# Kernel optimization log

Hardware: AMD Instinct MI355X
Metric: run time of the kernel (lower is better)

Reference implementation:

```python
import jax, jax.numpy as jnp
import numpy as np
import math

D = 1024      # d_model
K = 64        # k_eigenstates
H = 4         # n_heads
KH = K // H   # eigenstates per head
MLP = 4 * D
B, T = 4, 4096


def setup_inputs() -> dict:
    key = jax.random.key(0)
    ks = jax.random.split(key, 16)
    rn = lambda k, shape, s: (jax.random.normal(k, shape, jnp.float32) * s)
    inp = {
        "x": rn(ks[0], (B, T, D), 1.0),
        "W_in": rn(ks[1], (2 * K, D), 1.0 / math.sqrt(D)),
        "log_decay": jax.random.uniform(ks[2], (K,), jnp.float32, -3.0, -0.1),
        "frequency": jnp.linspace(0.0, 2 * math.pi * (1 - 1.0 / K), K, dtype=jnp.float32),
        "W_sel": rn(ks[3], (2 * K, D), 0.01 / math.sqrt(D)),
        "b_sel": jnp.zeros((2 * K,), jnp.float32),
        "R": jnp.eye(KH, dtype=jnp.float32)[None] + 0.01 * rn(ks[4], (H, KH, KH), 1.0 / math.sqrt(KH)),
        "W_out": rn(ks[5], (D, 2 * K), 1.0 / math.sqrt(2 * K)),
        "W_g": rn(ks[6], (D, D), 1.0 / math.sqrt(D)),
        "b_g": jnp.full((D,), -2.0, jnp.float32),
        "g1": jnp.ones((D,), jnp.float32),
        "be1": jnp.zeros((D,), jnp.float32),
        "g2": jnp.ones((D,), jnp.float32),
        "be2": jnp.zeros((D,), jnp.float32),
        "W1": rn(ks[7], (MLP, D), 1.0 / math.sqrt(D)),
        "b1": jnp.zeros((MLP,), jnp.float32),
        "W2": rn(ks[8], (D, MLP), 1.0 / math.sqrt(MLP)),
        "b2": jnp.zeros((D,), jnp.float32),
    }
    return inp


def _ln(x, g, b):
    m = jnp.mean(x, axis=-1, keepdims=True)
    v = jnp.mean(jnp.square(x - m), axis=-1, keepdims=True)
    return (x - m) * jax.lax.rsqrt(v + 1e-5) * g + b


def _scan_combine(e1, e2):
    a1, b1 = e1
    a2, b2 = e2
    return a1 * a2, a2 * b1 + b2


def reference(x, W_in, log_decay, frequency, W_sel, b_sel, R, W_out, W_g, b_g,
              g1, be1, g2, be2, W1, b1, W2, b2):
    Bsz, Ts, Dm = x.shape
    residual = x
    x_norm = _ln(x, g1, be1)

    beta = x_norm @ W_in.T                      # [B,T,2K]
    beta_r, beta_i = jnp.split(beta, 2, axis=-1)

    delta = x_norm @ W_sel.T + b_sel            # selective modulation
    d_dec, d_fr = jnp.split(delta, 2, axis=-1)
    mag = jax.nn.sigmoid(log_decay + 0.1 * jnp.tanh(d_dec))   # [B,T,K]
    freq = frequency + 0.05 * jnp.tanh(d_fr)

    a = jax.lax.complex(mag * jnp.cos(freq), mag * jnp.sin(freq))  # lambda_t
    bc = jax.lax.complex(beta_r, beta_i)
    # inclusive prefix scan of c_t = a_t * c_{t-1} + b_t
    _, c = jax.lax.associative_scan(_scan_combine, (a, bc), axis=1)
    c_r, c_i = c.real, c.imag                   # [B,T,K]

    nH, Kh = R.shape[0], R.shape[1]
    c_r = jnp.einsum('hjk,bthk->bthj', R, c_r.reshape(Bsz, Ts, nH, Kh)).reshape(Bsz, Ts, -1)
    c_i = jnp.einsum('hjk,bthk->bthj', R, c_i.reshape(Bsz, Ts, nH, Kh)).reshape(Bsz, Ts, -1)

    h = jnp.concatenate([c_r, c_i], axis=-1) @ W_out.T
    gate = jax.nn.sigmoid(x_norm @ W_g.T + b_g)
    x = residual + gate * h

    x2 = _ln(x, g2, be2)
    x = x + (jax.nn.silu(x2 @ W1.T + b1) @ W2.T + b2)
    return x
```

## Files before the change

### kernel.cpp

```cpp
#include <hip/hip_runtime.h>
#include <math.h>

typedef __bf16 bf16_t;
typedef __attribute__((ext_vector_type(8))) __bf16 bf16x8;
typedef __attribute__((ext_vector_type(4))) __bf16 bf16x4;
typedef __attribute__((ext_vector_type(4))) float f32x4;

#define DMODEL 1024
#define NROWS  16384
#define SEQLEN 4096

static __device__ __forceinline__ float sigmoidf_(float v) { return 1.f / (1.f + __expf(-v)); }
static __device__ __forceinline__ float tanhf_(float v) {
  v = fminf(fmaxf(v, -15.f), 15.f);
  float e = __expf(-2.f * v);
  return (1.f - e) / (1.f + e);
}

#define GLOAD16(gsrc, ldst) __builtin_amdgcn_global_load_lds(                     \
    (const __attribute__((address_space(1))) void*)(gsrc),                        \
    (__attribute__((address_space(3))) void*)(ldst), 16, 0, 0)

__global__ __launch_bounds__(256) void ln_fused_kernel(const float* __restrict__ x,
                                                       const float* __restrict__ g,
                                                       const float* __restrict__ b,
                                                       bf16_t* __restrict__ out) {
  int row = blockIdx.x;
  int tid = threadIdx.x;
  const float4* xr = (const float4*)(x + (size_t)row * DMODEL);
  float4 v = xr[tid];
  float s  = v.x + v.y + v.z + v.w;
  float s2 = v.x*v.x + v.y*v.y + v.z*v.z + v.w*v.w;
  #pragma unroll
  for (int off = 32; off > 0; off >>= 1) {
    s  += __shfl_down(s, off);
    s2 += __shfl_down(s2, off);
  }
  __shared__ float sh[4], sh2[4];
  int lane = tid & 63, wid = tid >> 6;
  if (lane == 0) { sh[wid] = s; sh2[wid] = s2; }
  __syncthreads();
  s  = sh[0] + sh[1] + sh[2] + sh[3];
  s2 = sh2[0] + sh2[1] + sh2[2] + sh2[3];
  float m = s * (1.f / DMODEL);
  float var = fmaxf(s2 * (1.f / DMODEL) - m * m, 0.f);
  float rs = rsqrtf(var + 1e-5f);
  float4 gv = *(const float4*)&g[tid * 4];
  float4 bv = *(const float4*)&b[tid * 4];
  union { bf16_t h[4]; float2 f2; } u;
  u.h[0] = (bf16_t)((v.x - m) * rs * gv.x + bv.x);
  u.h[1] = (bf16_t)((v.y - m) * rs * gv.y + bv.y);
  u.h[2] = (bf16_t)((v.z - m) * rs * gv.z + bv.z);
  u.h[3] = (bf16_t)((v.w - m) * rs * gv.w + bv.w);
  *(float2*)&out[(size_t)row * DMODEL + tid * 4] = u.f2;
}

__global__ __launch_bounds__(256) void ln_fused_bf16_kernel(const bf16_t* __restrict__ x,
                                                            const float* __restrict__ g,
                                                            const float* __restrict__ b,
                                                            bf16_t* __restrict__ out) {
  int row = blockIdx.x;
  int tid = threadIdx.x;
  bf16x4 hv = *(const bf16x4*)(x + (size_t)row * DMODEL + tid * 4);
  float v0 = (float)hv[0], v1 = (float)hv[1], v2 = (float)hv[2], v3 = (float)hv[3];
  float s  = v0 + v1 + v2 + v3;
  float s2 = v0*v0 + v1*v1 + v2*v2 + v3*v3;
  #pragma unroll
  for (int off = 32; off > 0; off >>= 1) {
    s  += __shfl_down(s, off);
    s2 += __shfl_down(s2, off);
  }
  __shared__ float sh[4], sh2[4];
  int lane = tid & 63, wid = tid >> 6;
  if (lane == 0) { sh[wid] = s; sh2[wid] = s2; }
  __syncthreads();
  s  = sh[0] + sh[1] + sh[2] + sh[3];
  s2 = sh2[0] + sh2[1] + sh2[2] + sh2[3];
  float m = s * (1.f / DMODEL);
  float var = fmaxf(s2 * (1.f / DMODEL) - m * m, 0.f);
  float rs = rsqrtf(var + 1e-5f);
  float4 gv = *(const float4*)&g[tid * 4];
  float4 bv = *(const float4*)&b[tid * 4];
  union { bf16_t h[4]; float2 f2; } u;
  u.h[0] = (bf16_t)((v0 - m) * rs * gv.x + bv.x);
  u.h[1] = (bf16_t)((v1 - m) * rs * gv.y + bv.y);
  u.h[2] = (bf16_t)((v2 - m) * rs * gv.z + bv.z);
  u.h[3] = (bf16_t)((v3 - m) * rs * gv.w + bv.w);
  *(float2*)&out[(size_t)row * DMODEL + tid * 4] = u.f2;
}

__global__ __launch_bounds__(256) void f32_to_bf16_kernel(const float* __restrict__ in,
                                                          bf16_t* __restrict__ out, int n) {
  int idx = (blockIdx.x * 256 + threadIdx.x) * 4;
  if (idx >= n) return;
  float4 v = *(const float4*)&in[idx];
  union { bf16_t h[4]; float2 f2; } u;
  u.h[0] = (bf16_t)v.x; u.h[1] = (bf16_t)v.y; u.h[2] = (bf16_t)v.z; u.h[3] = (bf16_t)v.w;
  *(float2*)&out[idx] = u.f2;
}

template<int EPI>
__global__ __launch_bounds__(512, 4) void gemmB_kernel(
    const bf16_t* __restrict__ A, int lda,
    const bf16_t* __restrict__ B, int ldb, int K, int nx,
    const float* __restrict__ bias,
    const float* __restrict__ resf,
    const bf16_t* __restrict__ resb,
    const bf16_t* __restrict__ auxb,
    float* __restrict__ outf, bf16_t* __restrict__ outb, int ldout) {
  __shared__ __align__(128) bf16_t Asm[128 * 64];
  __shared__ __align__(128) bf16_t Bsm[256 * 64];
  const int nwg = gridDim.x;
  const int bid = blockIdx.x;
  const int lid = (bid & 7) * (nwg >> 3) + (bid >> 3);
  const int n0 = (lid % nx) * 256;
  const int r0 = (lid / nx) * 128;

  const int tid = threadIdx.x;
  const int lane = tid & 63;
  const int w = tid >> 6;
  const int wr = w >> 2, wc = w & 3;
  const int fr = lane & 15;
  const int q16 = (lane >> 4) * 16;
  const int swz = (fr & 7) << 4;
  const int trow = tid >> 3;
  const int scolb = ((tid & 7) ^ (trow & 7)) << 4;

  const size_t lda_b = (size_t)lda * 2;
  const size_t ldb_b = (size_t)ldb * 2;
  const char* Ab = (const char*)A;
  const char* Bb = (const char*)B;
  char* lA = (char*)Asm;
  char* lB = (char*)Bsm;

  f32x4 acc[4][4];
  #pragma unroll
  for (int m = 0; m < 4; ++m)
    #pragma unroll
    for (int n = 0; n < 4; ++n) acc[m][n] = (f32x4){0.f, 0.f, 0.f, 0.f};

  for (int kt = 0; kt < K; kt += 64) {
    const char* sa = Ab + (size_t)(r0 + trow) * lda_b + kt * 2 + scolb;
    GLOAD16(sa, lA + tid * 16);
    GLOAD16(sa + 64 * lda_b, lA + 8192 + tid * 16);
    const char* sb = Bb + (size_t)(n0 + trow) * ldb_b + kt * 2 + scolb;
    GLOAD16(sb, lB + tid * 16);
    GLOAD16(sb + 64 * ldb_b,  lB + 8192  + tid * 16);
    GLOAD16(sb + 128 * ldb_b, lB + 16384 + tid * 16);
    GLOAD16(sb + 192 * ldb_b, lB + 24576 + tid * 16);
    __syncthreads();
    #pragma unroll
    for (int kh = 0; kh < 2; ++kh) {
      bf16x8 af[4], bv[4];
      #pragma unroll
      for (int m = 0; m < 4; ++m)
        af[m] = *(const bf16x8*)(lA + (wr * 64 + m * 16 + fr) * 128 + ((kh * 64 + q16) ^ swz));
      #pragma unroll
      for (int n = 0; n < 4; ++n)
        bv[n] = *(const bf16x8*)(lB + (wc * 64 + n * 16 + fr) * 128 + ((kh * 64 + q16) ^ swz));
      #pragma unroll
      for (int m = 0; m < 4; ++m)
        #pragma unroll
        for (int n = 0; n < 4; ++n)
          acc[m][n] = __builtin_amdgcn_mfma_f32_16x16x32_bf16(af[m], bv[n], acc[m][n], 0, 0, 0);
    }
    __syncthreads();
  }

  const int rbase = (lane >> 4) * 4;
  #pragma unroll
  for (int mf = 0; mf < 4; ++mf) {
    #pragma unroll
    for (int n = 0; n < 4; ++n) {
      int row = r0 + wr * 64 + mf * 16 + rbase;
      int col = n0 + wc * 64 + n * 16 + fr;
      f32x4 v = acc[mf][n];
      #pragma unroll
      for (int j = 0; j < 4; ++j) {
        int r = row + j;
        float val = v[j];
        if (EPI == 0) {
          outf[(size_t)r * ldout + col] = val;
        } else if (EPI == 1) {
          float t2 = val + bias[col];
          t2 = t2 * sigmoidf_(t2);
          outb[(size_t)r * ldout + col] = (bf16_t)t2;
        } else if (EPI == 2) {
          outf[(size_t)r * ldout + col] =
              (float)resb[(size_t)r * 1024 + col] + bias[col] + val;
        } else if (EPI == 3) {
          outf[(size_t)r * ldout + col] += val;
        } else if (EPI == 4) {
          size_t idx = (size_t)r * 1024 + col;
          outb[idx] = (bf16_t)(resf[idx] + sigmoidf_(val + bias[col]) * (float)auxb[idx]);
        } else {
          outb[(size_t)r * ldout + col] = (bf16_t)val;
        }
      }
    }
  }
}

template<int EPI>
__global__ __launch_bounds__(256) void gemm_bf16_kernel(
    const bf16_t* __restrict__ A, int lda,
    const bf16_t* __restrict__ B, int ldb, int K, int nx,
    float* __restrict__ outf, int ldout) {
  __shared__ __align__(16) bf16_t As[128 * 32];
  __shared__ __align__(16) bf16_t Bs[128 * 32];
  const int nwg = gridDim.x;
  const int bid = blockIdx.x;
  const int lid = (bid & 7) * (nwg >> 3) + (bid >> 3);
  const int n0 = (lid % nx) * 128;
  const int r0 = (lid / nx) * 128;

  const int tid = threadIdx.x;
  const int lane = tid & 63;
  const int w = tid >> 6;
  const int wr = w >> 1, wc = w & 1;
  const int srow0 = tid >> 2;
  const int srow1 = 64 + (tid >> 2);
  const int skk = (tid & 3) * 8;
  const int fr = lane & 15;
  const int ko = (lane >> 4) * 8;

  f32x4 acc[4][4];
  #pragma unroll
  for (int m = 0; m < 4; ++m)
    #pragma unroll
    for (int n = 0; n < 4; ++n) acc[m][n] = (f32x4){0.f, 0.f, 0.f, 0.f};

  for (int k0 = 0; k0 < K; k0 += 32) {
    GLOAD16(A + (size_t)(r0 + srow0) * lda + k0 + skk, (char*)As + w * 1024);
    GLOAD16(A + (size_t)(r0 + srow1) * lda + k0 + skk, (char*)As + 4096 + w * 1024);
    GLOAD16(B + (size_t)(n0 + srow0) * ldb + k0 + skk, (char*)Bs + w * 1024);
    GLOAD16(B + (size_t)(n0 + srow1) * ldb + k0 + skk, (char*)Bs + 4096 + w * 1024);
    __syncthreads();
    bf16x8 af[4], bfr[4];
    #pragma unroll
    for (int m = 0; m < 4; ++m)
      af[m] = *(const bf16x8*)&As[(wr * 64 + m * 16 + fr) * 32 + ko];
    #pragma unroll
    for (int n = 0; n < 4; ++n)
      bfr[n] = *(const bf16x8*)&Bs[(wc * 64 + n * 16 + fr) * 32 + ko];
    #pragma unroll
    for (int m = 0; m < 4; ++m)
      #pragma unroll
      for (int n = 0; n < 4; ++n)
        acc[m][n] = __builtin_amdgcn_mfma_f32_16x16x32_bf16(af[m], bfr[n], acc[m][n], 0, 0, 0);
    __syncthreads();
  }

  const int rbase = (lane >> 4) * 4;
  #pragma unroll
  for (int m = 0; m < 4; ++m) {
    #pragma unroll
    for (int n = 0; n < 4; ++n) {
      int row = r0 + wr * 64 + m * 16 + rbase;
      int col = n0 + wc * 64 + n * 16 + fr;
      f32x4 v = acc[m][n];
      #pragma unroll
      for (int j = 0; j < 4; ++j)
        outf[(size_t)(row + j) * ldout + col] = v[j];
    }
  }
}

__global__ __launch_bounds__(256) void scan_fused_kernel(
    const float* __restrict__ bdt,
    const float* __restrict__ log_decay, const float* __restrict__ frequency,
    const float* __restrict__ b_sel,
    float* __restrict__ c_r, float* __restrict__ c_i) {
  int seq = blockIdx.x;
  int bb = seq >> 6, k = seq & 63;
  int tid = threadIdx.x;
  size_t col = (size_t)bb * 4096 + tid * 16;
  const f32x4* pbr = (const f32x4*)(bdt + (size_t)k * 16384 + col);
  const f32x4* pbi = (const f32x4*)(bdt + (size_t)(64 + k) * 16384 + col);
  const f32x4* pdd = (const f32x4*)(bdt + (size_t)(128 + k) * 16384 + col);
  const f32x4* pdf = (const f32x4*)(bdt + (size_t)(192 + k) * 16384 + col);
  const float ld = log_decay[k], fq = frequency[k];
  const float bsd = b_sel[k], bsf = b_sel[64 + k];

  float arv[16], aiv[16], brv[16], biv[16];
  float Ar = 1.f, Ai = 0.f, Br = 0.f, Bi = 0.f;
  #pragma unroll
  for (int g = 0; g < 4; ++g) {
    f32x4 vbr = pbr[g], vbi = pbi[g], vdd = pdd[g], vdf = pdf[g];
    #pragma unroll
    for (int j = 0; j < 4; ++j) {
      int s = g * 4 + j;
      float mag = sigmoidf_(ld + 0.1f * tanhf_(vdd[j] + bsd));
      float f = fq + 0.05f * tanhf_(vdf[j] + bsf);
      float sn, cs;
      __sincosf(f, &sn, &cs);
      float ar = mag * cs, ai = mag * sn;
      float br = vbr[j], bi = vbi[j];
      arv[s] = ar; aiv[s] = ai; brv[s] = br; biv[s] = bi;
      float nBr = ar * Br - ai * Bi + br;
      float nBi = ar * Bi + ai * Br + bi;
      Br = nBr; Bi = nBi;
      float nAr = ar * Ar - ai * Ai;
      float nAi = ar * Ai + ai * Ar;
      Ar = nAr; Ai = nAi;
    }
  }

  __shared__ float sAr[256], sAi[256], sBr[256], sBi[256];
  sAr[tid] = Ar; sAi[tid] = Ai; sBr[tid] = Br; sBi[tid] = Bi;
  for (int off = 1; off < 256; off <<= 1) {
    __syncthreads();
    float pAr = 0.f, pAi = 0.f, pBr = 0.f, pBi = 0.f;
    if (tid >= off) { pAr = sAr[tid - off]; pAi = sAi[tid - off]; pBr = sBr[tid - off]; pBi = sBi[tid - off]; }
    __syncthreads();
    if (tid >= off) {
      float cAr = sAr[tid], cAi = sAi[tid], cBr = sBr[tid], cBi = sBi[tid];
      float nBr = cAr * pBr - cAi * pBi + cBr;
      float nBi = cAr * pBi + cAi * pBr + cBi;
      float nAr = cAr * pAr - cAi * pAi;
      float nAi = cAr * pAi + cAi * pAr;
      sAr[tid] = nAr; sAi[tid] = nAi; sBr[tid] = nBr; sBi[tid] = nBi;
    }
  }
  __syncthreads();
  float cr = (tid > 0) ? sBr[tid - 1] : 0.f;
  float ci = (tid > 0) ? sBi[tid - 1] : 0.f;

  float* outr = c_r + (size_t)seq * 4096 + tid * 16;
  float* outi = c_i + (size_t)seq * 4096 + tid * 16;
  #pragma unroll
  for (int g = 0; g < 4; ++g) {
    f32x4 vr, vi;
    #pragma unroll
    for (int j = 0; j < 4; ++j) {
      int s = g * 4 + j;
      float nr = arv[s] * cr - aiv[s] * ci + brv[s];
      float ni = arv[s] * ci + aiv[s] * cr + biv[s];
      cr = nr; ci = ni;
      vr[j] = cr; vi[j] = ci;
    }
    *(f32x4*)(outr + g * 4) = vr;
    *(f32x4*)(outi + g * 4) = vi;
  }
}

__global__ __launch_bounds__(256) void transpose_cc_kernel(
    const float* __restrict__ c_r, const float* __restrict__ c_i,
    bf16_t* __restrict__ cc) {
  __shared__ float Tr[64][65];
  __shared__ float Ti[64][65];
  int t0 = blockIdx.x * 64;
  int bb = blockIdx.y;
  int tid = threadIdx.x;
  int tt = tid & 63;
  int q = tid >> 6;
  #pragma unroll
  for (int p = 0; p < 16; ++p) {
    int k = p * 4 + q;
    size_t src = ((size_t)bb * 64 + k) * 4096 + t0 + tt;
    Tr[tt][k] = c_r[src];
    Ti[tt][k] = c_i[src];
  }
  __syncthreads();
  #pragma unroll
  for (int p = 0; p < 16; ++p) {
    int tt2 = p * 4 + q;
    int k = tid & 63;
    size_t row = (size_t)bb * 4096 + t0 + tt2;
    cc[row * 128 + k] = (bf16_t)Tr[tt2][k];
    cc[row * 128 + 64 + k] = (bf16_t)Ti[tt2][k];
  }
}

__global__ __launch_bounds__(256) void weff_kernel(const float* __restrict__ W_out,
                                                   const float* __restrict__ R,
                                                   bf16_t* __restrict__ Weff) {
  int idx = blockIdx.x * 256 + threadIdx.x;
  int d = idx >> 7, col = idx & 127;
  int k = col & 63, h = k >> 4, kk = k & 15;
  int off = (col < 64) ? 0 : 64;
  float s = 0.f;
  #pragma unroll
  for (int j = 0; j < 16; ++j)
    s += W_out[d * 128 + off + h * 16 + j] * R[h * 256 + j * 16 + kk];
  Weff[idx] = (bf16_t)s;
}

extern "C" void kernel_launch(void* const* d_in, const int* in_sizes, int n_in,
                              void* d_out, int out_size, void* d_ws, size_t ws_size,
                              hipStream_t stream) {
  (void)in_sizes; (void)n_in; (void)out_size;
  const float* x         = (const float*)d_in[0];
  const float* W_in      = (const float*)d_in[1];
  const float* log_decay = (const float*)d_in[2];
  const float* frequency = (const float*)d_in[3];
  const float* W_sel     = (const float*)d_in[4];
  const float* b_sel     = (const float*)d_in[5];
  const float* R         = (const float*)d_in[6];
  const float* W_out     = (const float*)d_in[7];
  const float* W_g       = (const float*)d_in[8];
  const float* b_g       = (const float*)d_in[9];
  const float* g1        = (const float*)d_in[10];
  const float* be1       = (const float*)d_in[11];
  const float* g2        = (const float*)d_in[12];
  const float* be2       = (const float*)d_in[13];
  const float* W1        = (const float*)d_in[14];
  const float* b1        = (const float*)d_in[15];
  const float* W2        = (const float*)d_in[16];
  const float* b2        = (const float*)d_in[17];
  float* out = (float*)d_out;
  float* ws  = (float*)d_ws;

  const size_t M1 = (size_t)1 << 20;
  const bool full = ws_size >= (size_t)61 * M1 * sizeof(float);

  float* bd_t = ws;
  float* c_r  = ws + 4 * M1;
  float* c_i  = ws + 8 * M1;
  bf16_t* cc  = (bf16_t*)(ws + 12 * M1);
  bf16_t* mid = (bf16_t*)ws;
  size_t o = full ? 32 * M1 : 16 * M1;
  bf16_t* xmid  = (bf16_t*)(ws + o);
  bf16_t* hbufb = (bf16_t*)(ws + o + 8 * M1);
  bf16_t* xn    = (bf16_t*)(ws + o + 16 * M1);
  size_t wb = o + 24 * M1;
  bf16_t* Wbd = (bf16_t*)(ws + wb);
  bf16_t* Wgb = (bf16_t*)(ws + wb + (128 << 10));
  bf16_t* W1b = (bf16_t*)(ws + wb + (640 << 10));
  bf16_t* W2b = (bf16_t*)(ws + wb + 2 * M1 + (640 << 10));
  bf16_t* Wef = (bf16_t*)(ws + wb + 4 * M1 + (640 << 10));

  dim3 blk(256);
  dim3 blk512(512);

  ln_fused_kernel<<<NROWS, blk, 0, stream>>>(x, g1, be1, xn);

  f32_to_bf16_kernel<<<128, blk, 0, stream>>>(W_in, Wbd, 128 * 1024);
  f32_to_bf16_kernel<<<128, blk, 0, stream>>>(W_sel, Wbd + 128 * 1024, 128 * 1024);
  f32_to_bf16_kernel<<<1024, blk, 0, stream>>>(W_g, Wgb, 1024 * 1024);
  f32_to_bf16_kernel<<<4096, blk, 0, stream>>>(W1, W1b, 4 * 1024 * 1024);
  f32_to_bf16_kernel<<<4096, blk, 0, stream>>>(W2, W2b, 4 * 1024 * 1024);
  weff_kernel<<<512, blk, 0, stream>>>(W_out, R, Wef);

  gemm_bf16_kernel<0><<<256, blk, 0, stream>>>(Wbd, 1024, xn, 1024, 1024, 128, bd_t, 16384);

  scan_fused_kernel<<<256, blk, 0, stream>>>(bd_t, log_decay, frequency, b_sel, c_r, c_i);

  transpose_cc_kernel<<<dim3(64, 4), blk, 0, stream>>>(c_r, c_i, cc);

  gemmB_kernel<5><<<512, blk512, 0, stream>>>(
      cc, 128, Wef, 128, 128, 4, nullptr, nullptr, nullptr, nullptr, nullptr, hbufb, 1024);

  gemmB_kernel<4><<<512, blk512, 0, stream>>>(
      xn, 1024, Wgb, 1024, 1024, 4, b_g, x, nullptr, hbufb, nullptr, xmid, 1024);

  ln_fused_bf16_kernel<<<NROWS, blk, 0, stream>>>(xmid, g2, be2, xn);

  if (full) {
    gemmB_kernel<1><<<2048, blk512, 0, stream>>>(
        xn, 1024, W1b, 1024, 1024, 16, b1, nullptr, nullptr, nullptr, nullptr, mid, 4096);
    gemmB_kernel<2><<<512, blk512, 0, stream>>>(
        mid, 4096, W2b, 4096, 4096, 4, b2, nullptr, xmid, nullptr, out, nullptr, 1024);
  } else {
    for (int h = 0; h < 2; ++h) {
      gemmB_kernel<1><<<1024, blk512, 0, stream>>>(
          xn, 1024, W1b + (size_t)h * 2048 * 1024, 1024, 1024, 8,
          b1 + h * 2048, nullptr, nullptr, nullptr, nullptr, mid, 2048);
      if (h == 0) {
        gemmB_kernel<2><<<512, blk512, 0, stream>>>(
            mid, 2048, W2b, 4096, 2048, 4, b2, nullptr, xmid, nullptr, out, nullptr, 1024);
      } else {
        gemmB_kernel<3><<<512, blk512, 0, stream>>>(
            mid, 2048, W2b + 2048, 4096, 2048, 4, nullptr, nullptr, nullptr, nullptr, out, nullptr, 1024);
      }
    }
  }
}
```

Before: 446.2 us.

## Fuse output projection into gate GEMM and merge weight conversions

The output-projection GEMM (cc @ Wef) and the gate GEMM are merged into one kernel that keeps two accumulator sets and applies the residual+sigmoid gate epilogue directly. This removes the bf16 h buffer write and read round trip and one kernel launch. The five weight fp32-to-bf16 conversion launches are also merged into one launch over a contiguous destination. Holding two 4x4 accumulator arrays raises register pressure, which could reduce occupancy, and h is no longer rounded to bf16 before the gate.

```diff
diff --git a/kernel.cpp b/kernel.cpp
--- a/kernel.cpp
+++ b/kernel.cpp
@@ -89,14 +89,23 @@
   *(float2*)&out[(size_t)row * DMODEL + tid * 4] = u.f2;
 }
 
-__global__ __launch_bounds__(256) void f32_to_bf16_kernel(const float* __restrict__ in,
-                                                          bf16_t* __restrict__ out, int n) {
-  int idx = (blockIdx.x * 256 + threadIdx.x) * 4;
-  if (idx >= n) return;
-  float4 v = *(const float4*)&in[idx];
+__global__ __launch_bounds__(256) void conv_all_kernel(
+    const float* __restrict__ W_in, const float* __restrict__ W_sel,
+    const float* __restrict__ W_g, const float* __restrict__ W1,
+    const float* __restrict__ W2, bf16_t* __restrict__ dstb) {
+  int q = blockIdx.x * 256 + threadIdx.x;
+  size_t e = (size_t)q * 4;
+  const float* src;
+  size_t off;
+  if (e < 131072)        { src = W_in;  off = e; }
+  else if (e < 262144)   { src = W_sel; off = e - 131072; }
+  else if (e < 1310720)  { src = W_g;   off = e - 262144; }
+  else if (e < 5505024)  { src = W1;    off = e - 1310720; }
+  else                   { src = W2;    off = e - 5505024; }
+  float4 v = *(const float4*)&src[off];
   union { bf16_t h[4]; float2 f2; } u;
   u.h[0] = (bf16_t)v.x; u.h[1] = (bf16_t)v.y; u.h[2] = (bf16_t)v.z; u.h[3] = (bf16_t)v.w;
-  *(float2*)&out[idx] = u.f2;
+  *(float2*)&dstb[e] = u.f2;
 }
 
 template<int EPI>
@@ -104,9 +113,7 @@
     const bf16_t* __restrict__ A, int lda,
     const bf16_t* __restrict__ B, int ldb, int K, int nx,
     const float* __restrict__ bias,
-    const float* __restrict__ resf,
     const bf16_t* __restrict__ resb,
-    const bf16_t* __restrict__ auxb,
     float* __restrict__ outf, bf16_t* __restrict__ outb, int ldout) {
   __shared__ __align__(128) bf16_t Asm[128 * 64];
   __shared__ __align__(128) bf16_t Bsm[256 * 64];
@@ -190,12 +197,115 @@
               (float)resb[(size_t)r * 1024 + col] + bias[col] + val;
         } else if (EPI == 3) {
           outf[(size_t)r * ldout + col] += val;
-        } else if (EPI == 4) {
-          size_t idx = (size_t)r * 1024 + col;
-          outb[idx] = (bf16_t)(resf[idx] + sigmoidf_(val + bias[col]) * (float)auxb[idx]);
         } else {
           outb[(size_t)r * ldout + col] = (bf16_t)val;
         }
+      }
+    }
+  }
+}
+
+__global__ __launch_bounds__(512, 4) void gateh_kernel(
+    const bf16_t* __restrict__ xn, const bf16_t* __restrict__ Wg,
+    const bf16_t* __restrict__ cc, const bf16_t* __restrict__ Wef,
+    const float* __restrict__ x, const float* __restrict__ b_g,
+    bf16_t* __restrict__ xmid) {
+  __shared__ __align__(128) bf16_t Asm[128 * 64];
+  __shared__ __align__(128) bf16_t Bsm[256 * 64];
+  const int nwg = gridDim.x;
+  const int bid = blockIdx.x;
+  const int lid = (bid & 7) * (nwg >> 3) + (bid >> 3);
+  const int n0 = (lid & 3) * 256;
+  const int r0 = (lid >> 2) * 128;
+
+  const int tid = threadIdx.x;
+  const int lane = tid & 63;
+  const int w = tid >> 6;
+  const int wr = w >> 2, wc = w & 3;
+  const int fr = lane & 15;
+  const int q16 = (lane >> 4) * 16;
+  const int swz = (fr & 7) << 4;
+  const int trow = tid >> 3;
+  const int scolb = ((tid & 7) ^ (trow & 7)) << 4;
+  char* lA = (char*)Asm;
+  char* lB = (char*)Bsm;
+
+  f32x4 accg[4][4], acch[4][4];
+  #pragma unroll
+  for (int m = 0; m < 4; ++m)
+    #pragma unroll
+    for (int n = 0; n < 4; ++n) {
+      accg[m][n] = (f32x4){0.f, 0.f, 0.f, 0.f};
+      acch[m][n] = (f32x4){0.f, 0.f, 0.f, 0.f};
+    }
+
+  for (int kt = 0; kt < 1024; kt += 64) {
+    const char* sa = (const char*)xn + (size_t)(r0 + trow) * 2048 + kt * 2 + scolb;
+    GLOAD16(sa, lA + tid * 16);
+    GLOAD16(sa + 64 * 2048, lA + 8192 + tid * 16);
+    const char* sb = (const char*)Wg + (size_t)(n0 + trow) * 2048 + kt * 2 + scolb;
+    GLOAD16(sb, lB + tid * 16);
+    GLOAD16(sb + 64 * 2048,  lB + 8192  + tid * 16);
+    GLOAD16(sb + 128 * 2048, lB + 16384 + tid * 16);
+    GLOAD16(sb + 192 * 2048, lB + 24576 + tid * 16);
+    __syncthreads();
+    #pragma unroll
+    for (int kh = 0; kh < 2; ++kh) {
+      bf16x8 af[4], bv[4];
+      #pragma unroll
+      for (int m = 0; m < 4; ++m)
+        af[m] = *(const bf16x8*)(lA + (wr * 64 + m * 16 + fr) * 128 + ((kh * 64 + q16) ^ swz));
+      #pragma unroll
+      for (int n = 0; n < 4; ++n)
+        bv[n] = *(const bf16x8*)(lB + (wc * 64 + n * 16 + fr) * 128 + ((kh * 64 + q16) ^ swz));
+      #pragma unroll
+      for (int m = 0; m < 4; ++m)
+        #pragma unroll
+        for (int n = 0; n < 4; ++n)
+          accg[m][n] = __builtin_amdgcn_mfma_f32_16x16x32_bf16(af[m], bv[n], accg[m][n], 0, 0, 0);
+    }
+    __syncthreads();
+  }
+
+  for (int kt = 0; kt < 128; kt += 64) {
+    const char* sa = (const char*)cc + (size_t)(r0 + trow) * 256 + kt * 2 + scolb;
+    GLOAD16(sa, lA + tid * 16);
+    GLOAD16(sa + 64 * 256, lA + 8192 + tid * 16);
+    const char* sb = (const char*)Wef + (size_t)(n0 + trow) * 256 + kt * 2 + scolb;
+    GLOAD16(sb, lB + tid * 16);
+    GLOAD16(sb + 64 * 256,  lB + 8192  + tid * 16);
+    GLOAD16(sb + 128 * 256, lB + 16384 + tid * 16);
+    GLOAD16(sb + 192 * 256, lB + 24576 + tid * 16);
+    __syncthreads();
+    #pragma unroll
+    for (int kh = 0; kh < 2; ++kh) {
+      bf16x8 af[4], bv[4];
+      #pragma unroll
+      for (int m = 0; m < 4; ++m)
+        af[m] = *(const bf16x8*)(lA + (wr * 64 + m * 16 + fr) * 128 + ((kh * 64 + q16) ^ swz));
+      #pragma unroll
+      for (int n = 0; n < 4; ++n)
+        bv[n] = *(const bf16x8*)(lB + (wc * 64 + n * 16 + fr) * 128 + ((kh * 64 + q16) ^ swz));
+      #pragma unroll
+      for (int m = 0; m < 4; ++m)
+        #pragma unroll
+        for (int n = 0; n < 4; ++n)
+          acch[m][n] = __builtin_amdgcn_mfma_f32_16x16x32_bf16(af[m], bv[n], acch[m][n], 0, 0, 0);
+    }
+    __syncthreads();
+  }
+
+  const int rbase = (lane >> 4) * 4;
+  #pragma unroll
+  for (int mf = 0; mf < 4; ++mf) {
+    #pragma unroll
+    for (int n = 0; n < 4; ++n) {
+      int row = r0 + wr * 64 + mf * 16 + rbase;
+      int col = n0 + wc * 64 + n * 16 + fr;
+      #pragma unroll
+      for (int j = 0; j < 4; ++j) {
+        size_t idx = (size_t)(row + j) * 1024 + col;
+        xmid[idx] = (bf16_t)(x[idx] + sigmoidf_(accg[mf][n][j] + b_g[col]) * acch[mf][n][j]);
       }
     }
   }
@@ -421,25 +531,20 @@
   bf16_t* mid = (bf16_t*)ws;
   size_t o = full ? 32 * M1 : 16 * M1;
   bf16_t* xmid  = (bf16_t*)(ws + o);
-  bf16_t* hbufb = (bf16_t*)(ws + o + 8 * M1);
-  bf16_t* xn    = (bf16_t*)(ws + o + 16 * M1);
-  size_t wb = o + 24 * M1;
+  bf16_t* xn    = (bf16_t*)(ws + o + 8 * M1);
+  size_t wb = o + 16 * M1;
   bf16_t* Wbd = (bf16_t*)(ws + wb);
-  bf16_t* Wgb = (bf16_t*)(ws + wb + (128 << 10));
-  bf16_t* W1b = (bf16_t*)(ws + wb + (640 << 10));
-  bf16_t* W2b = (bf16_t*)(ws + wb + 2 * M1 + (640 << 10));
-  bf16_t* Wef = (bf16_t*)(ws + wb + 4 * M1 + (640 << 10));
+  bf16_t* Wgb = Wbd + 262144;
+  bf16_t* W1b = Wgb + 1048576;
+  bf16_t* W2b = W1b + 4194304;
+  bf16_t* Wef = W2b + 4194304;
 
   dim3 blk(256);
   dim3 blk512(512);
 
   ln_fused_kernel<<<NROWS, blk, 0, stream>>>(x, g1, be1, xn);
 
-  f32_to_bf16_kernel<<<128, blk, 0, stream>>>(W_in, Wbd, 128 * 1024);
-  f32_to_bf16_kernel<<<128, blk, 0, stream>>>(W_sel, Wbd + 128 * 1024, 128 * 1024);
-  f32_to_bf16_kernel<<<1024, blk, 0, stream>>>(W_g, Wgb, 1024 * 1024);
-  f32_to_bf16_kernel<<<4096, blk, 0, stream>>>(W1, W1b, 4 * 1024 * 1024);
-  f32_to_bf16_kernel<<<4096, blk, 0, stream>>>(W2, W2b, 4 * 1024 * 1024);
+  conv_all_kernel<<<9472, blk, 0, stream>>>(W_in, W_sel, W_g, W1, W2, Wbd);
   weff_kernel<<<512, blk, 0, stream>>>(W_out, R, Wef);
 
   gemm_bf16_kernel<0><<<256, blk, 0, stream>>>(Wbd, 1024, xn, 1024, 1024, 128, bd_t, 16384);
@@ -448,30 +553,26 @@
 
   transpose_cc_kernel<<<dim3(64, 4), blk, 0, stream>>>(c_r, c_i, cc);
 
-  gemmB_kernel<5><<<512, blk512, 0, stream>>>(
-      cc, 128, Wef, 128, 128, 4, nullptr, nullptr, nullptr, nullptr, nullptr, hbufb, 1024);
-
-  gemmB_kernel<4><<<512, blk512, 0, stream>>>(
-      xn, 1024, Wgb, 1024, 1024, 4, b_g, x, nullptr, hbufb, nullptr, xmid, 1024);
+  gateh_kernel<<<512, blk512, 0, stream>>>(xn, Wgb, cc, Wef, x, b_g, xmid);
 
   ln_fused_bf16_kernel<<<NROWS, blk, 0, stream>>>(xmid, g2, be2, xn);
 
   if (full) {
     gemmB_kernel<1><<<2048, blk512, 0, stream>>>(
-        xn, 1024, W1b, 1024, 1024, 16, b1, nullptr, nullptr, nullptr, nullptr, mid, 4096);
+        xn, 1024, W1b, 1024, 1024, 16, b1, nullptr, nullptr, mid, 4096);
     gemmB_kernel<2><<<512, blk512, 0, stream>>>(
-        mid, 4096, W2b, 4096, 4096, 4, b2, nullptr, xmid, nullptr, out, nullptr, 1024);
+        mid, 4096, W2b, 4096, 4096, 4, b2, xmid, out, nullptr, 1024);
   } else {
     for (int h = 0; h < 2; ++h) {
       gemmB_kernel<1><<<1024, blk512, 0, stream>>>(
           xn, 1024, W1b + (size_t)h * 2048 * 1024, 1024, 1024, 8,
-          b1 + h * 2048, nullptr, nullptr, nullptr, nullptr, mid, 2048);
+          b1 + h * 2048, nullptr, nullptr, mid, 2048);
       if (h == 0) {
         gemmB_kernel<2><<<512, blk512, 0, stream>>>(
-            mid, 2048, W2b, 4096, 2048, 4, b2, nullptr, xmid, nullptr, out, nullptr, 1024);
+            mid, 2048, W2b, 4096, 2048, 4, b2, xmid, out, nullptr, 1024);
       } else {
         gemmB_kernel<3><<<512, blk512, 0, stream>>>(
-            mid, 2048, W2b + 2048, 4096, 2048, 4, nullptr, nullptr, nullptr, nullptr, out, nullptr, 1024);
+            mid, 2048, W2b + 2048, 4096, 2048, 4, nullptr, nullptr, out, nullptr, 1024);
       }
     }
   }
```

Measured after the change: 498.3 us. 1.12x slower.
